# Kernel tuning notes

Measured on AMD Instinct MI355X. Metric: run time of the kernel, lower is better.

The kernel has to match this reference:

```python
import jax, jax.numpy as jnp
import numpy as np
import math

B, T, D = 4, 2048, 1024
H = 16            # n_heads
HD = D // H       # head_dim = 64
LAT = 128         # latent_dim
ROPE = 32         # rope_dim
EPS = 1e-6


def rms_norm(x, g):
    rms = jnp.sqrt(jnp.mean(x * x, axis=-1, keepdims=True) + EPS)
    return g * (x / rms)


def setup_inputs() -> dict:
    key = jax.random.key(0)
    ks = jax.random.split(key, 7)
    s = lambda fan_in: 1.0 / math.sqrt(fan_in)
    x = jax.random.normal(ks[0], (B, T, D), dtype=jnp.float32)
    Wq = jax.random.normal(ks[1], (D, D), dtype=jnp.float32) * s(D)
    Wkv = jax.random.normal(ks[2], (D, LAT), dtype=jnp.float32) * s(D)
    Wk = jax.random.normal(ks[3], (LAT, H * ROPE), dtype=jnp.float32) * s(LAT)
    Wv = jax.random.normal(ks[4], (LAT, H * (HD - ROPE)), dtype=jnp.float32) * s(LAT)
    Wo = jax.random.normal(ks[5], (D, D), dtype=jnp.float32) * s(D)
    q_g = jnp.ones((HD,), dtype=jnp.float32)
    k_g = jnp.ones((ROPE,), dtype=jnp.float32)
    return {"x": x, "Wq": Wq, "Wkv": Wkv, "Wk": Wk, "Wv": Wv, "Wo": Wo,
            "q_g": q_g, "k_g": k_g}


def reference(x, Wq, Wkv, Wk, Wv, Wo, q_g, k_g):
    b, t, d = x.shape
    # Q projection -> (b, h, t, hd), RMSNorm over head_dim
    q = (x @ Wq).reshape(b, t, H, HD).transpose(0, 2, 1, 3)
    q = rms_norm(q, q_g)
    # KV latent compression
    kv = x @ Wkv                                   # (b, t, LAT)
    k = (kv @ Wk).reshape(b, t, H, ROPE).transpose(0, 2, 1, 3)   # (b,h,t,rope)
    k = rms_norm(k, k_g)
    v_c = (kv @ Wv).reshape(b, t, H, HD - ROPE).transpose(0, 2, 1, 3)
    # K is zero-padded to head_dim, so only the first ROPE dims of q contribute
    scores = jnp.einsum('bhtr,bhsr->bhts', q[..., :ROPE], k) / math.sqrt(HD)
    causal = jnp.triu(jnp.ones((t, t), dtype=bool), k=1)
    scores = jnp.where(causal, -jnp.inf, scores)
    probs = jax.nn.softmax(scores, axis=-1)        # (b, h, t, s)
    # V is zero-padded at the end by ROPE dims -> compute then pad
    out_c = jnp.einsum('bhts,bhsd->bhtd', probs, v_c)   # (b,h,t,HD-ROPE)
    out = jnp.pad(out_c, ((0, 0), (0, 0), (0, 0), (0, ROPE)))
    out = out.transpose(0, 2, 1, 3).reshape(b, t, d)
    return out @ Wo
```

## Files before the change

kernel.cpp:

```cpp
#include <hip/hip_runtime.h>
#include <hip/hip_bf16.h>
#include <math.h>

using bf16 = __hip_bfloat16;
typedef __attribute__((ext_vector_type(8))) short bf16x8;
typedef __attribute__((ext_vector_type(4))) float f32x4;

#define BB   4
#define TT   2048
#define DD   1024
#define HH   16
#define HD_  64
#define LAT_ 128
#define RP   32
#define EPS_ 1e-6f

static __device__ __forceinline__ void stf(float* p, float v) { *p = v; }
static __device__ __forceinline__ void stf(bf16* p, float v) { *p = __float2bfloat16(v); }

static __device__ __forceinline__ void gl2lds16(const void* g, void* l)
{
    __builtin_amdgcn_global_load_lds(
        (const __attribute__((address_space(1))) void*)g,
        (__attribute__((address_space(3))) void*)l, 16, 0, 0);
}

__global__ __launch_bounds__(256)
void sentinel_kernel(float* __restrict__ out, float val, long long n)
{
    long long i = (long long)blockIdx.x * 256 + threadIdx.x;
    if (i < n) out[i] = val;
}

__global__ __launch_bounds__(256)
void conv_x_kernel(const float* __restrict__ x, bf16* __restrict__ xb, long long n4)
{
    long long i = (long long)blockIdx.x * 256 + threadIdx.x;
    if (i >= n4) return;
    float4 v = *(const float4*)(x + i * 4);
    union { bf16 h[4]; uint2 u; } o;
    o.h[0] = __float2bfloat16(v.x);
    o.h[1] = __float2bfloat16(v.y);
    o.h[2] = __float2bfloat16(v.z);
    o.h[3] = __float2bfloat16(v.w);
    *(uint2*)(xb + i * 4) = o.u;
}

__global__ __launch_bounds__(256)
void conv_trans_kernel(const float* __restrict__ W, bf16* __restrict__ WT,
                       int K, int N)
{
    __shared__ __align__(16) bf16 t[64][72];
    const int k0 = blockIdx.y * 64, n0 = blockIdx.x * 64;
    const int tid = threadIdx.x;
    const int r = tid >> 2, c0 = (tid & 3) * 16;
    const float* src = W + (size_t)(k0 + r) * N + n0 + c0;
    #pragma unroll
    for (int j = 0; j < 16; j += 4) {
        float4 v = *(const float4*)(src + j);
        t[c0 + j + 0][r] = __float2bfloat16(v.x);
        t[c0 + j + 1][r] = __float2bfloat16(v.y);
        t[c0 + j + 2][r] = __float2bfloat16(v.z);
        t[c0 + j + 3][r] = __float2bfloat16(v.w);
    }
    __syncthreads();
    const int rr = tid >> 2, cc = (tid & 3) * 16;
    bf16* dst = WT + (size_t)(n0 + rr) * K + k0 + cc;
    *(bf16x8*)dst       = *(const bf16x8*)&t[rr][cc];
    *(bf16x8*)(dst + 8) = *(const bf16x8*)&t[rr][cc + 8];
}

__global__ __launch_bounds__(256)
void conv_wkwv_kernel(const float* __restrict__ Wk, const float* __restrict__ Wv,
                      bf16* __restrict__ WT)
{
    int idx = blockIdx.x * 256 + threadIdx.x;
    if (idx >= 128 * 1024) return;
    int k = idx >> 10, n = idx & 1023;
    float v = (n < 512) ? Wk[k * 512 + n] : Wv[k * 512 + (n - 512)];
    WT[(size_t)n * 128 + k] = __float2bfloat16(v);
}

__global__ __launch_bounds__(256)
void conv_woT_kernel(const float* __restrict__ Wo, bf16* __restrict__ WT)
{
    __shared__ __align__(16) bf16 t[64][72];
    const int mm0 = blockIdx.y * 64, n0 = blockIdx.x * 64;
    const int tid = threadIdx.x;
    const int r = tid >> 2, c0 = (tid & 3) * 16;
    const int mm = mm0 + r;
    const int row = ((mm >> 5) << 6) | (mm & 31);
    const float* src = Wo + (size_t)row * 1024 + n0 + c0;
    #pragma unroll
    for (int j = 0; j < 16; j += 4) {
        float4 v = *(const float4*)(src + j);
        t[c0 + j + 0][r] = __float2bfloat16(v.x);
        t[c0 + j + 1][r] = __float2bfloat16(v.y);
        t[c0 + j + 2][r] = __float2bfloat16(v.z);
        t[c0 + j + 3][r] = __float2bfloat16(v.w);
    }
    __syncthreads();
    const int rr = tid >> 2, cc = (tid & 3) * 16;
    bf16* dst = WT + (size_t)(n0 + rr) * 512 + mm0 + cc;
    *(bf16x8*)dst       = *(const bf16x8*)&t[rr][cc];
    *(bf16x8*)(dst + 8) = *(const bf16x8*)&t[rr][cc + 8];
}

#define GEMM_PROLOG_128 \
    __shared__ __align__(16) short As[128][32]; \
    __shared__ __align__(16) short Bs[128][32]; \
    const int tid  = threadIdx.x; \
    const int wave = tid >> 6, lane = tid & 63; \
    const int quad = lane >> 4, l16 = lane & 15; \
    const int wr = (wave >> 1) * 64, wc = (wave & 1) * 64; \
    const int row0 = blockIdx.y * 128, col0 = blockIdx.x * 128; \
    const int srow = tid >> 2, scol = (tid & 3) * 8; \
    char* lAs0 = (char*)As + wave * 1024; \
    char* lAs1 = (char*)As + 4096 + wave * 1024; \
    char* lBs0 = (char*)Bs + wave * 1024; \
    char* lBs1 = (char*)Bs + 4096 + wave * 1024; \
    f32x4 acc[4][4]; \
    _Pragma("unroll") \
    for (int mt = 0; mt < 4; ++mt) \
        _Pragma("unroll") \
        for (int nt = 0; nt < 4; ++nt) \
            acc[mt][nt] = (f32x4){0.f, 0.f, 0.f, 0.f}; \
    for (int k0 = 0; k0 < K; k0 += 32) { \
        const short* ga = A  + (size_t)(row0 + srow) * K + k0 + scol; \
        const short* gb = BT + (size_t)(col0 + srow) * K + k0 + scol; \
        __syncthreads(); \
        gl2lds16(ga,                  lAs0); \
        gl2lds16(ga + (size_t)64 * K, lAs1); \
        gl2lds16(gb,                  lBs0); \
        gl2lds16(gb + (size_t)64 * K, lBs1); \
        __syncthreads(); \
        bf16x8 af[4], bfv[4]; \
        _Pragma("unroll") \
        for (int mt = 0; mt < 4; ++mt) \
            af[mt] = *(const bf16x8*)&As[wr + mt * 16 + l16][quad * 8]; \
        _Pragma("unroll") \
        for (int nt = 0; nt < 4; ++nt) \
            bfv[nt] = *(const bf16x8*)&Bs[wc + nt * 16 + l16][quad * 8]; \
        _Pragma("unroll") \
        for (int mt = 0; mt < 4; ++mt) \
            _Pragma("unroll") \
            for (int nt = 0; nt < 4; ++nt) \
                acc[mt][nt] = __builtin_amdgcn_mfma_f32_16x16x32_bf16( \
                    af[mt], bfv[nt], acc[mt][nt], 0, 0, 0); \
    }

template <typename OT>
__global__ __launch_bounds__(256)
void gemm_mfma(const short* __restrict__ A, const short* __restrict__ BT,
               OT* __restrict__ C, int M, int N, int K)
{
    GEMM_PROLOG_128
    #pragma unroll
    for (int mt = 0; mt < 4; ++mt)
        #pragma unroll
        for (int nt = 0; nt < 4; ++nt) {
            const int col = col0 + wc + nt * 16 + l16;
            #pragma unroll
            for (int r = 0; r < 4; ++r) {
                const int row = row0 + wr + mt * 16 + quad * 4 + r;
                stf(C + (size_t)row * N + col, acc[mt][nt][r]);
            }
        }
}

__global__ __launch_bounds__(256)
void gemm_qrms(const short* __restrict__ A, const short* __restrict__ BT,
               bf16* __restrict__ qn, const float* __restrict__ qg,
               int M, int N, int K)
{
    GEMM_PROLOG_128
    const int h = (col0 + wc) >> 6;
    const float g0 = qg[l16], g1 = qg[16 + l16];
    #pragma unroll
    for (int mt = 0; mt < 4; ++mt) {
        float ss[4];
        #pragma unroll
        for (int r = 0; r < 4; ++r)
            ss[r] = acc[mt][0][r] * acc[mt][0][r] + acc[mt][1][r] * acc[mt][1][r]
                  + acc[mt][2][r] * acc[mt][2][r] + acc[mt][3][r] * acc[mt][3][r];
        #pragma unroll
        for (int off = 1; off < 16; off <<= 1)
            #pragma unroll
            for (int r = 0; r < 4; ++r) ss[r] += __shfl_xor(ss[r], off, 64);
        #pragma unroll
        for (int r = 0; r < 4; ++r) {
            const float inv = 0.125f / sqrtf(ss[r] * (1.0f / HD_) + EPS_);
            const int row = row0 + wr + mt * 16 + quad * 4 + r;
            const int b = row >> 11, t = row & 2047;
            bf16* op = qn + (((size_t)(b * HH + h)) * TT + t) * RP;
            op[l16]      = __float2bfloat16(g0 * acc[mt][0][r] * inv);
            op[16 + l16] = __float2bfloat16(g1 * acc[mt][1][r] * inv);
        }
    }
}

__global__ __launch_bounds__(256)
void gemm_kv(const short* __restrict__ A, const short* __restrict__ BT,
             bf16* __restrict__ kn, bf16* __restrict__ vb,
             const float* __restrict__ kg, int M, int N, int K)
{
    GEMM_PROLOG_128
    const int colbase = col0 + wc;
    if (colbase < 512) {
        const int h0 = colbase >> 5;
        const float g0 = kg[l16], g1 = kg[16 + l16];
        #pragma unroll
        for (int mt = 0; mt < 4; ++mt) {
            float s0[4], s1[4];
            #pragma unroll
            for (int r = 0; r < 4; ++r) {
                s0[r] = acc[mt][0][r] * acc[mt][0][r] + acc[mt][1][r] * acc[mt][1][r];
                s1[r] = acc[mt][2][r] * acc[mt][2][r] + acc[mt][3][r] * acc[mt][3][r];
            }
            #pragma unroll
            for (int off = 1; off < 16; off <<= 1)
                #pragma unroll
                for (int r = 0; r < 4; ++r) {
                    s0[r] += __shfl_xor(s0[r], off, 64);
                    s1[r] += __shfl_xor(s1[r], off, 64);
                }
            #pragma unroll
            for (int r = 0; r < 4; ++r) {
                const float i0 = 1.0f / sqrtf(s0[r] * (1.0f / RP) + EPS_);
                const float i1 = 1.0f / sqrtf(s1[r] * (1.0f / RP) + EPS_);
                const int row = row0 + wr + mt * 16 + quad * 4 + r;
                const int b = row >> 11, t = row & 2047;
                bf16* op0 = kn + (((size_t)(b * HH + h0)) * TT + t) * RP;
                bf16* op1 = kn + (((size_t)(b * HH + h0 + 1)) * TT + t) * RP;
                op0[l16]      = __float2bfloat16(g0 * acc[mt][0][r] * i0);
                op0[16 + l16] = __float2bfloat16(g1 * acc[mt][1][r] * i0);
                op1[l16]      = __float2bfloat16(g0 * acc[mt][2][r] * i1);
                op1[16 + l16] = __float2bfloat16(g1 * acc[mt][3][r] * i1);
            }
        }
    } else {
        const int h0 = (colbase - 512) >> 5;
        #pragma unroll
        for (int mt = 0; mt < 4; ++mt)
            #pragma unroll
            for (int r = 0; r < 4; ++r) {
                const int row = row0 + wr + mt * 16 + quad * 4 + r;
                const int b = row >> 11, t = row & 2047;
                bf16* op0 = vb + (((size_t)(b * HH + h0)) * TT + t) * RP;
                bf16* op1 = vb + (((size_t)(b * HH + h0 + 1)) * TT + t) * RP;
                op0[l16]      = __float2bfloat16(acc[mt][0][r]);
                op0[16 + l16] = __float2bfloat16(acc[mt][1][r]);
                op1[l16]      = __float2bfloat16(acc[mt][2][r]);
                op1[16 + l16] = __float2bfloat16(acc[mt][3][r]);
            }
    }
}

__global__ __launch_bounds__(256)
void gemm_k64(const short* __restrict__ A, const short* __restrict__ BT,
              bf16* __restrict__ C, int M, int N, int K)
{
    __shared__ __align__(16) short As[64][32];
    __shared__ __align__(16) short Bs[128][32];
    const int tid  = threadIdx.x;
    const int wave = tid >> 6, lane = tid & 63;
    const int quad = lane >> 4, l16 = lane & 15;
    const int wr = (wave >> 1) * 32, wc = (wave & 1) * 64;
    const int row0 = blockIdx.y * 64, col0 = blockIdx.x * 128;
    const int srow = tid >> 2, scol = (tid & 3) * 8;

    char* lAs  = (char*)As + wave * 1024;
    char* lBs0 = (char*)Bs + wave * 1024;
    char* lBs1 = (char*)Bs + 4096 + wave * 1024;

    f32x4 acc[2][4];
    #pragma unroll
    for (int mt = 0; mt < 2; ++mt)
        #pragma unroll
        for (int nt = 0; nt < 4; ++nt)
            acc[mt][nt] = (f32x4){0.f, 0.f, 0.f, 0.f};

    for (int k0 = 0; k0 < K; k0 += 32) {
        const short* ga = A  + (size_t)(row0 + srow) * K + k0 + scol;
        const short* gb = BT + (size_t)(col0 + srow) * K + k0 + scol;
        __syncthreads();
        gl2lds16(ga,                  lAs);
        gl2lds16(gb,                  lBs0);
        gl2lds16(gb + (size_t)64 * K, lBs1);
        __syncthreads();

        bf16x8 af[2], bfv[4];
        #pragma unroll
        for (int mt = 0; mt < 2; ++mt)
            af[mt] = *(const bf16x8*)&As[wr + mt * 16 + l16][quad * 8];
        #pragma unroll
        for (int nt = 0; nt < 4; ++nt)
            bfv[nt] = *(const bf16x8*)&Bs[wc + nt * 16 + l16][quad * 8];
        #pragma unroll
        for (int mt = 0; mt < 2; ++mt)
            #pragma unroll
            for (int nt = 0; nt < 4; ++nt)
                acc[mt][nt] = __builtin_amdgcn_mfma_f32_16x16x32_bf16(
                    af[mt], bfv[nt], acc[mt][nt], 0, 0, 0);
    }

    #pragma unroll
    for (int mt = 0; mt < 2; ++mt)
        #pragma unroll
        for (int nt = 0; nt < 4; ++nt) {
            const int col = col0 + wc + nt * 16 + l16;
            #pragma unroll
            for (int r = 0; r < 4; ++r) {
                const int row = row0 + wr + mt * 16 + quad * 4 + r;
                C[(size_t)row * N + col] = __float2bfloat16(acc[mt][nt][r]);
            }
        }
}

__global__ __launch_bounds__(256)
void vtrans_kernel(const bf16* __restrict__ vb, bf16* __restrict__ vT)
{
    __shared__ __align__(16) short tile[32][72];
    const int bh = blockIdx.y;
    const int t0 = blockIdx.x * 64;
    const int tid = threadIdx.x;
    const int tl = tid >> 2, c0 = (tid & 3) * 8;
    bf16x8 v = *(const bf16x8*)(vb + ((size_t)bh * TT + t0 + tl) * RP + c0);
    #pragma unroll
    for (int j = 0; j < 8; ++j) tile[c0 + j][tl] = v[j];
    __syncthreads();
    const int c = tid >> 3, tt = (tid & 7) * 8;
    bf16x8 o = *(const bf16x8*)&tile[c][tt];
    *(bf16x8*)(vT + ((size_t)bh * RP + c) * TT + t0 + tt) = o;
}

struct __attribute__((aligned(8))) bf4 { bf16 v[4]; };

__global__ __launch_bounds__(512, 4)
void attn_mfma(const bf16* __restrict__ qn, const bf16* __restrict__ kn,
               const bf16* __restrict__ vT, bf16* __restrict__ att)
{
    __shared__ __align__(16) short KsF[2][64 * 32];
    __shared__ __align__(16) short VsF[2][32 * 64];
    __shared__ __align__(16) bf16 P_lds[8][16][72];
    const int tid  = threadIdx.x;
    const int w8   = tid >> 6, lane = tid & 63;
    const int quad = lane >> 4, l16 = lane & 15;
    const int f  = (int)(blockIdx.y * 8 + blockIdx.x);
    const int xr = f & 7, j = f >> 3;
    const int bx = j & 7;
    const int bh = xr + 8 * (j >> 3);
    const int b = bh >> 4, h = bh & 15;

    const bf16* knb = kn + (size_t)bh * TT * RP;
    const bf16* vtb = vT + (size_t)bh * RP * TT;

    const bool isK = (w8 < 4);
    const int  cK = tid;
    const int  cV = tid - 256;
    const bf16* sBase = isK
        ? knb + (size_t)(cK >> 2) * RP + ((cK & 3) ^ ((cK >> 3) & 3)) * 8
        : vtb + (size_t)(cV >> 3) * TT + ((cV & 7) ^ ((cV >> 3) & 7)) * 8;
    const long long sStep = (long long)(isK ? RP : 1) * 64;
    const int ldsOff = isK ? w8 * 1024 : (w8 - 4) * 1024;

    const int kslot = ((l16 >> 1) & 3);
    const int vswz  = (l16 & 7);

    #pragma unroll 1
    for (int pi = 0; pi < 2; ++pi) {
        const int qt = pi ? (15 - bx) : bx;
        const int NT = 2 * qt + 2;
        const int qbase = qt * 128 + w8 * 16;

        if (pi) {
            asm volatile("s_waitcnt vmcnt(0)\n\ts_barrier" ::: "memory");
        }

        bf16x8 qf = *(const bf16x8*)(qn + ((size_t)bh * TT + qbase + l16) * RP + quad * 8);

        float lsum = 0.f;
        f32x4 oacc0 = (f32x4){0.f, 0.f, 0.f, 0.f};
        f32x4 oacc1 = (f32x4){0.f, 0.f, 0.f, 0.f};

        gl2lds16(sBase, (isK ? (char*)KsF[0] : (char*)VsF[0]) + ldsOff);
        int cur = 0;

        for (int st = 0; st < NT; ++st) {
            asm volatile("s_waitcnt vmcnt(0)\n\ts_barrier" ::: "memory");

            const int nxt = cur ^ 1;
            gl2lds16(sBase + (long long)(st + 1) * sStep,
                     (isK ? (char*)KsF[nxt] : (char*)VsF[nxt]) + ldsOff);

            const int s0 = st * 64;
            const short* KsC = KsF[cur];
            const short* VsC = VsF[cur];

            f32x4 sc[4];
            #pragma unroll
            for (int sub = 0; sub < 4; ++sub) {
                bf16x8 kf = *(const bf16x8*)&KsC[(sub * 16 + l16) * 32
                                                 + ((quad ^ kslot) * 8)];
                sc[sub] = __builtin_amdgcn_mfma_f32_16x16x32_bf16(
                    kf, qf, (f32x4){0.f, 0.f, 0.f, 0.f}, 0, 0, 0);
            }

            if (s0 + 63 > qbase) {
                const int qg_ = qbase + l16;
                #pragma unroll
                for (int sub = 0; sub < 4; ++sub)
                    #pragma unroll
                    for (int r = 0; r < 4; ++r)
                        if (s0 + sub * 16 + quad * 4 + r > qg_) sc[sub][r] = -1e30f;
            }

            #pragma unroll
            for (int sub = 0; sub < 4; ++sub) {
                const float p0 = __expf(sc[sub][0]);
                const float p1 = __expf(sc[sub][1]);
                const float p2 = __expf(sc[sub][2]);
                const float p3 = __expf(sc[sub][3]);
                bf4 pk;
                pk.v[0] = __float2bfloat16(p0);
                pk.v[1] = __float2bfloat16(p1);
                pk.v[2] = __float2bfloat16(p2);
                pk.v[3] = __float2bfloat16(p3);
                *(bf4*)&P_lds[w8][l16][sub * 16 + quad * 4] = pk;
                lsum += (p0 + p1) + (p2 + p3);
            }

            #pragma unroll
            for (int ks = 0; ks < 2; ++ks) {
                bf16x8 pf  = *(const bf16x8*)&P_lds[w8][l16][ks * 32 + quad * 8];
                bf16x8 vf0 = *(const bf16x8*)&VsC[l16 * 64
                                + (((ks * 4 + quad) ^ vswz) * 8)];
                bf16x8 vf1 = *(const bf16x8*)&VsC[(16 + l16) * 64
                                + (((ks * 4 + quad) ^ vswz) * 8)];
                oacc0 = __builtin_amdgcn_mfma_f32_16x16x32_bf16(pf, vf0, oacc0, 0, 0, 0);
                oacc1 = __builtin_amdgcn_mfma_f32_16x16x32_bf16(pf, vf1, oacc1, 0, 0, 0);
            }

            cur = nxt;
        }

        lsum += __shfl_xor(lsum, 16, 64);
        lsum += __shfl_xor(lsum, 32, 64);
        #pragma unroll
        for (int r = 0; r < 4; ++r) {
            const float ls = __shfl(lsum, quad * 20 + r, 64);
            const float inv = 1.0f / ls;
            const int t = qbase + quad * 4 + r;
            bf16* op = att + ((size_t)(b * TT + t)) * 512 + h * 32;
            op[l16]      = __float2bfloat16(oacc0[r] * inv);
            op[16 + l16] = __float2bfloat16(oacc1[r] * inv);
        }
    }
}

extern "C" void kernel_launch(void* const* d_in, const int* in_sizes, int n_in,
                              void* d_out, int out_size, void* d_ws, size_t ws_size,
                              hipStream_t stream)
{
    float* out = (float*)d_out;
    const long long NOUT = (long long)BB * TT * DD;
    const int outgrid = (int)((NOUT + 255) / 256);

    static const long long expect[8] =
        {8388608, 1048576, 131072, 65536, 65536, 1048576, 64, 32};
    if (n_in != 8) {
        sentinel_kernel<<<outgrid, 256, 0, stream>>>(out, 20000.0f + 100.0f * n_in, NOUT);
        return;
    }
    for (int i = 0; i < 8; ++i) {
        if ((long long)in_sizes[i] != expect[i]) {
            sentinel_kernel<<<outgrid, 256, 0, stream>>>(out, 10000.0f + 1000.0f * i, NOUT);
            return;
        }
    }
    if (ws_size < 62914624ULL) {
        sentinel_kernel<<<outgrid, 256, 0, stream>>>(
            out, 30000.0f + (float)(ws_size >> 20), NOUT);
        return;
    }
    if (out_size != 8388608) {
        sentinel_kernel<<<outgrid, 256, 0, stream>>>(
            out, 512.0f * (1.0f + (float)(out_size >> 20)), NOUT);
        return;
    }

    const float* x   = (const float*)d_in[0];
    const float* Wq  = (const float*)d_in[1];
    const float* Wkv = (const float*)d_in[2];
    const float* Wk  = (const float*)d_in[3];
    const float* Wv  = (const float*)d_in[4];
    const float* Wo  = (const float*)d_in[5];
    const float* qg  = (const float*)d_in[6];
    const float* kg  = (const float*)d_in[7];

    char* base = (char*)d_ws + 64;
    bf16*  xb    = (bf16*)(base + 0);
    bf16*  wqT   = (bf16*)(base + 16777216);
    bf16*  wkvT  = (bf16*)(base + 18874368);
    bf16*  kvb   = (bf16*)(base + 19136512);
    bf16*  att_b = (bf16*)(base + 0);
    bf16*  vTb   = (bf16*)(base + 8388608);
    bf16*  qn    = (bf16*)(base + 35913728);
    bf16*  kn    = (bf16*)(base + 44302336);
    bf16*  vb    = (bf16*)(base + 52690944);
    bf16*  wkwvT = (bf16*)(base + 61079552);
    bf16*  woT   = (bf16*)(base + 61341696);

    const int BT = BB * TT;

    conv_x_kernel<<<outgrid / 4, 256, 0, stream>>>(x, xb, NOUT / 4);
    conv_trans_kernel<<<dim3(16, 16), 256, 0, stream>>>(Wq, wqT, 1024, 1024);
    conv_trans_kernel<<<dim3(2, 16), 256, 0, stream>>>(Wkv, wkvT, 1024, 128);
    conv_wkwv_kernel<<<512, 256, 0, stream>>>(Wk, Wv, wkwvT);
    conv_woT_kernel<<<dim3(16, 8), 256, 0, stream>>>(Wo, woT);

    gemm_qrms<<<dim3(8, 64), 256, 0, stream>>>(
        (const short*)xb, (const short*)wqT, qn, qg, BT, DD, DD);
    gemm_k64<<<dim3(1, 128), 256, 0, stream>>>(
        (const short*)xb, (const short*)wkvT, kvb, BT, LAT_, DD);
    gemm_kv<<<dim3(8, 64), 256, 0, stream>>>(
        (const short*)kvb, (const short*)wkwvT, kn, vb, kg, BT, 2 * 512, LAT_);
    vtrans_kernel<<<dim3(32, 64), 256, 0, stream>>>(vb, vTb);
    attn_mfma<<<dim3(8, 64), 512, 0, stream>>>(qn, kn, vTb, att_b);
    gemm_mfma<float><<<dim3(8, 64), 256, 0, stream>>>(
        (const short*)att_b, (const short*)woT, out, BT, DD, 512);
}
```

Baseline: 230.2 us.

## Fuse V transpose into gemm_kv epilogue and share K/V tiles across paired query tiles

The gemm_kv epilogue now writes V straight into the transposed layout with packed 4-element stores, which removes the separate vtrans kernel and its extra round trip through memory. The attention kernel now handles its two paired query tiles in a single pass over the K/V stream instead of two sequential passes, so each K/V tile loaded into LDS serves both tiles and the second prologue and barrier go away. The Q scale now folds in log2(e), so exp2f replaces __expf. The cost is more live registers for the two sets of accumulators and query fragments, and strided 8-byte V stores.

```diff
diff --git a/kernel.cpp b/kernel.cpp
--- a/kernel.cpp
+++ b/kernel.cpp
@@ -14,6 +14,7 @@
 #define LAT_ 128
 #define RP   32
 #define EPS_ 1e-6f
+#define QSCALE_ 0.18033688011112042f
 
 static __device__ __forceinline__ void stf(float* p, float v) { *p = v; }
 static __device__ __forceinline__ void stf(bf16* p, float v) { *p = __float2bfloat16(v); }
@@ -189,7 +190,7 @@
             for (int r = 0; r < 4; ++r) ss[r] += __shfl_xor(ss[r], off, 64);
         #pragma unroll
         for (int r = 0; r < 4; ++r) {
-            const float inv = 0.125f / sqrtf(ss[r] * (1.0f / HD_) + EPS_);
+            const float inv = QSCALE_ / sqrtf(ss[r] * (1.0f / HD_) + EPS_);
             const int row = row0 + wr + mt * 16 + quad * 4 + r;
             const int b = row >> 11, t = row & 2047;
             bf16* op = qn + (((size_t)(b * HH + h)) * TT + t) * RP;
@@ -199,9 +200,11 @@
     }
 }
 
+struct __attribute__((aligned(8))) bf4 { bf16 v[4]; };
+
 __global__ __launch_bounds__(256)
 void gemm_kv(const short* __restrict__ A, const short* __restrict__ BT,
-             bf16* __restrict__ kn, bf16* __restrict__ vb,
+             bf16* __restrict__ kn, bf16* __restrict__ vT,
              const float* __restrict__ kg, int M, int N, int K)
 {
     GEMM_PROLOG_128
@@ -243,15 +246,16 @@
         #pragma unroll
         for (int mt = 0; mt < 4; ++mt)
             #pragma unroll
-            for (int r = 0; r < 4; ++r) {
-                const int row = row0 + wr + mt * 16 + quad * 4 + r;
+            for (int nt = 0; nt < 4; ++nt) {
+                const int h = h0 + (nt >> 1);
+                const int c = (nt & 1) * 16 + l16;
+                const int row = row0 + wr + mt * 16 + quad * 4;
                 const int b = row >> 11, t = row & 2047;
-                bf16* op0 = vb + (((size_t)(b * HH + h0)) * TT + t) * RP;
-                bf16* op1 = vb + (((size_t)(b * HH + h0 + 1)) * TT + t) * RP;
-                op0[l16]      = __float2bfloat16(acc[mt][0][r]);
-                op0[16 + l16] = __float2bfloat16(acc[mt][1][r]);
-                op1[l16]      = __float2bfloat16(acc[mt][2][r]);
-                op1[16 + l16] = __float2bfloat16(acc[mt][3][r]);
+                bf4 pk;
+                #pragma unroll
+                for (int r = 0; r < 4; ++r)
+                    pk.v[r] = __float2bfloat16(acc[mt][nt][r]);
+                *(bf4*)(vT + (((size_t)(b * HH + h)) * RP + c) * TT + t) = pk;
             }
     }
 }
@@ -317,24 +321,65 @@
         }
 }
 
-__global__ __launch_bounds__(256)
-void vtrans_kernel(const bf16* __restrict__ vb, bf16* __restrict__ vT)
-{
-    __shared__ __align__(16) short tile[32][72];
-    const int bh = blockIdx.y;
-    const int t0 = blockIdx.x * 64;
-    const int tid = threadIdx.x;
-    const int tl = tid >> 2, c0 = (tid & 3) * 8;
-    bf16x8 v = *(const bf16x8*)(vb + ((size_t)bh * TT + t0 + tl) * RP + c0);
-    #pragma unroll
-    for (int j = 0; j < 8; ++j) tile[c0 + j][tl] = v[j];
-    __syncthreads();
-    const int c = tid >> 3, tt = (tid & 7) * 8;
-    bf16x8 o = *(const bf16x8*)&tile[c][tt];
-    *(bf16x8*)(vT + ((size_t)bh * RP + c) * TT + t0 + tt) = o;
-}
-
-struct __attribute__((aligned(8))) bf4 { bf16 v[4]; };
+#define ATTN_TILE(QF, QB, LSUM, OA, OB)                                         \
+    {                                                                           \
+        f32x4 sc[4];                                                            \
+        _Pragma("unroll")                                                       \
+        for (int sub = 0; sub < 4; ++sub) {                                     \
+            bf16x8 kf = *(const bf16x8*)&KsC[(sub * 16 + l16) * 32              \
+                                             + ((quad ^ kslot) * 8)];           \
+            sc[sub] = __builtin_amdgcn_mfma_f32_16x16x32_bf16(                  \
+                kf, QF, (f32x4){0.f, 0.f, 0.f, 0.f}, 0, 0, 0);                  \
+        }                                                                       \
+        if (s0 + 63 > (QB)) {                                                   \
+            const int qg_ = (QB) + l16;                                         \
+            _Pragma("unroll")                                                   \
+            for (int sub = 0; sub < 4; ++sub)                                   \
+                _Pragma("unroll")                                               \
+                for (int r = 0; r < 4; ++r)                                     \
+                    if (s0 + sub * 16 + quad * 4 + r > qg_) sc[sub][r] = -1e30f;\
+        }                                                                       \
+        _Pragma("unroll")                                                       \
+        for (int sub = 0; sub < 4; ++sub) {                                     \
+            const float p0 = exp2f(sc[sub][0]);                                 \
+            const float p1 = exp2f(sc[sub][1]);                                 \
+            const float p2 = exp2f(sc[sub][2]);                                 \
+            const float p3 = exp2f(sc[sub][3]);                                 \
+            bf4 pk;                                                             \
+            pk.v[0] = __float2bfloat16(p0);                                     \
+            pk.v[1] = __float2bfloat16(p1);                                     \
+            pk.v[2] = __float2bfloat16(p2);                                     \
+            pk.v[3] = __float2bfloat16(p3);                                     \
+            *(bf4*)&P_lds[w8][l16][sub * 16 + quad * 4] = pk;                   \
+            LSUM += (p0 + p1) + (p2 + p3);                                      \
+        }                                                                       \
+        _Pragma("unroll")                                                       \
+        for (int ks = 0; ks < 2; ++ks) {                                        \
+            bf16x8 pf  = *(const bf16x8*)&P_lds[w8][l16][ks * 32 + quad * 8];   \
+            bf16x8 vf0 = *(const bf16x8*)&VsC[l16 * 64                          \
+                            + (((ks * 4 + quad) ^ vswz) * 8)];                  \
+            bf16x8 vf1 = *(const bf16x8*)&VsC[(16 + l16) * 64                   \
+                            + (((ks * 4 + quad) ^ vswz) * 8)];                  \
+            OA = __builtin_amdgcn_mfma_f32_16x16x32_bf16(pf, vf0, OA, 0, 0, 0); \
+            OB = __builtin_amdgcn_mfma_f32_16x16x32_bf16(pf, vf1, OB, 0, 0, 0); \
+        }                                                                       \
+    }
+
+#define ATTN_EPI(QB, LSUM, OA, OB)                                              \
+    {                                                                           \
+        float ls_ = (LSUM);                                                     \
+        ls_ += __shfl_xor(ls_, 16, 64);                                         \
+        ls_ += __shfl_xor(ls_, 32, 64);                                         \
+        _Pragma("unroll")                                                       \
+        for (int r = 0; r < 4; ++r) {                                           \
+            const float lr  = __shfl(ls_, quad * 20 + r, 64);                   \
+            const float inv = 1.0f / lr;                                        \
+            const int t = (QB) + quad * 4 + r;                                  \
+            bf16* op = att + ((size_t)(b * TT + t)) * 512 + h * 32;             \
+            op[l16]      = __float2bfloat16((OA)[r] * inv);                     \
+            op[16 + l16] = __float2bfloat16((OB)[r] * inv);                     \
+        }                                                                       \
+    }
 
 __global__ __launch_bounds__(512, 4)
 void attn_mfma(const bf16* __restrict__ qn, const bf16* __restrict__ kn,
@@ -367,95 +412,42 @@
     const int kslot = ((l16 >> 1) & 3);
     const int vswz  = (l16 & 7);
 
-    #pragma unroll 1
-    for (int pi = 0; pi < 2; ++pi) {
-        const int qt = pi ? (15 - bx) : bx;
-        const int NT = 2 * qt + 2;
-        const int qbase = qt * 128 + w8 * 16;
-
-        if (pi) {
-            asm volatile("s_waitcnt vmcnt(0)\n\ts_barrier" ::: "memory");
+    const int NTA = 2 * bx + 2, NTB = 32 - 2 * bx;
+    const int qbaseA = bx * 128 + w8 * 16;
+    const int qbaseB = (15 - bx) * 128 + w8 * 16;
+
+    bf16x8 qfA = *(const bf16x8*)(qn + ((size_t)bh * TT + qbaseA + l16) * RP + quad * 8);
+    bf16x8 qfB = *(const bf16x8*)(qn + ((size_t)bh * TT + qbaseB + l16) * RP + quad * 8);
+
+    float lsumA = 0.f, lsumB = 0.f;
+    f32x4 oA0 = (f32x4){0.f, 0.f, 0.f, 0.f};
+    f32x4 oA1 = (f32x4){0.f, 0.f, 0.f, 0.f};
+    f32x4 oB0 = (f32x4){0.f, 0.f, 0.f, 0.f};
+    f32x4 oB1 = (f32x4){0.f, 0.f, 0.f, 0.f};
+
+    gl2lds16(sBase, (isK ? (char*)KsF[0] : (char*)VsF[0]) + ldsOff);
+    int cur = 0;
+
+    for (int st = 0; st < NTB; ++st) {
+        asm volatile("s_waitcnt vmcnt(0)\n\ts_barrier" ::: "memory");
+
+        const int nxt = cur ^ 1;
+        gl2lds16(sBase + (long long)(st + 1) * sStep,
+                 (isK ? (char*)KsF[nxt] : (char*)VsF[nxt]) + ldsOff);
+
+        const int s0 = st * 64;
+        const short* KsC = KsF[cur];
+        const short* VsC = VsF[cur];
+
+        ATTN_TILE(qfB, qbaseB, lsumB, oB0, oB1)
+        if (st < NTA) {
+            ATTN_TILE(qfA, qbaseA, lsumA, oA0, oA1)
         }
-
-        bf16x8 qf = *(const bf16x8*)(qn + ((size_t)bh * TT + qbase + l16) * RP + quad * 8);
-
-        float lsum = 0.f;
-        f32x4 oacc0 = (f32x4){0.f, 0.f, 0.f, 0.f};
-        f32x4 oacc1 = (f32x4){0.f, 0.f, 0.f, 0.f};
-
-        gl2lds16(sBase, (isK ? (char*)KsF[0] : (char*)VsF[0]) + ldsOff);
-        int cur = 0;
-
-        for (int st = 0; st < NT; ++st) {
-            asm volatile("s_waitcnt vmcnt(0)\n\ts_barrier" ::: "memory");
-
-            const int nxt = cur ^ 1;
-            gl2lds16(sBase + (long long)(st + 1) * sStep,
-                     (isK ? (char*)KsF[nxt] : (char*)VsF[nxt]) + ldsOff);
-
-            const int s0 = st * 64;
-            const short* KsC = KsF[cur];
-            const short* VsC = VsF[cur];
-
-            f32x4 sc[4];
-            #pragma unroll
-            for (int sub = 0; sub < 4; ++sub) {
-                bf16x8 kf = *(const bf16x8*)&KsC[(sub * 16 + l16) * 32
-                                                 + ((quad ^ kslot) * 8)];
-                sc[sub] = __builtin_amdgcn_mfma_f32_16x16x32_bf16(
-                    kf, qf, (f32x4){0.f, 0.f, 0.f, 0.f}, 0, 0, 0);
-            }
-
-            if (s0 + 63 > qbase) {
-                const int qg_ = qbase + l16;
-                #pragma unroll
-                for (int sub = 0; sub < 4; ++sub)
-                    #pragma unroll
-                    for (int r = 0; r < 4; ++r)
-                        if (s0 + sub * 16 + quad * 4 + r > qg_) sc[sub][r] = -1e30f;
-            }
-
-            #pragma unroll
-            for (int sub = 0; sub < 4; ++sub) {
-                const float p0 = __expf(sc[sub][0]);
-                const float p1 = __expf(sc[sub][1]);
-                const float p2 = __expf(sc[sub][2]);
-                const float p3 = __expf(sc[sub][3]);
-                bf4 pk;
-                pk.v[0] = __float2bfloat16(p0);
-                pk.v[1] = __float2bfloat16(p1);
-                pk.v[2] = __float2bfloat16(p2);
-                pk.v[3] = __float2bfloat16(p3);
-                *(bf4*)&P_lds[w8][l16][sub * 16 + quad * 4] = pk;
-                lsum += (p0 + p1) + (p2 + p3);
-            }
-
-            #pragma unroll
-            for (int ks = 0; ks < 2; ++ks) {
-                bf16x8 pf  = *(const bf16x8*)&P_lds[w8][l16][ks * 32 + quad * 8];
-                bf16x8 vf0 = *(const bf16x8*)&VsC[l16 * 64
-                                + (((ks * 4 + quad) ^ vswz) * 8)];
-                bf16x8 vf1 = *(const bf16x8*)&VsC[(16 + l16) * 64
-                                + (((ks * 4 + quad) ^ vswz) * 8)];
-                oacc0 = __builtin_amdgcn_mfma_f32_16x16x32_bf16(pf, vf0, oacc0, 0, 0, 0);
-                oacc1 = __builtin_amdgcn_mfma_f32_16x16x32_bf16(pf, vf1, oacc1, 0, 0, 0);
-            }
-
-            cur = nxt;
-        }
-
-        lsum += __shfl_xor(lsum, 16, 64);
-        lsum += __shfl_xor(lsum, 32, 64);
-        #pragma unroll
-        for (int r = 0; r < 4; ++r) {
-            const float ls = __shfl(lsum, quad * 20 + r, 64);
-            const float inv = 1.0f / ls;
-            const int t = qbase + quad * 4 + r;
-            bf16* op = att + ((size_t)(b * TT + t)) * 512 + h * 32;
-            op[l16]      = __float2bfloat16(oacc0[r] * inv);
-            op[16 + l16] = __float2bfloat16(oacc1[r] * inv);
-        }
-    }
+        cur = nxt;
+    }
+
+    ATTN_EPI(qbaseA, lsumA, oA0, oA1)
+    ATTN_EPI(qbaseB, lsumB, oB0, oB1)
 }
 
 extern "C" void kernel_launch(void* const* d_in, const int* in_sizes, int n_in,
@@ -507,7 +499,6 @@
     bf16*  vTb   = (bf16*)(base + 8388608);
     bf16*  qn    = (bf16*)(base + 35913728);
     bf16*  kn    = (bf16*)(base + 44302336);
-    bf16*  vb    = (bf16*)(base + 52690944);
     bf16*  wkwvT = (bf16*)(base + 61079552);
     bf16*  woT   = (bf16*)(base + 61341696);
 
@@ -524,8 +515,7 @@
     gemm_k64<<<dim3(1, 128), 256, 0, stream>>>(
         (const short*)xb, (const short*)wkvT, kvb, BT, LAT_, DD);
     gemm_kv<<<dim3(8, 64), 256, 0, stream>>>(
-        (const short*)kvb, (const short*)wkwvT, kn, vb, kg, BT, 2 * 512, LAT_);
-    vtrans_kernel<<<dim3(32, 64), 256, 0, stream>>>(vb, vTb);
+        (const short*)kvb, (const short*)wkwvT, kn, vTb, kg, BT, 2 * 512, LAT_);
     attn_mfma<<<dim3(8, 64), 512, 0, stream>>>(qn, kn, vTb, att_b);
     gemm_mfma<float><<<dim3(8, 64), 256, 0, stream>>>(
         (const short*)att_b, (const short*)woT, out, BT, DD, 512);
```

New measurement: 238.4 us. 1.04x slower.
